# Optimization experiments

Measured on AMD Instinct MI355X. Metric: run time of the kernel, lower is better.

The kernel has to match this reference:

```python
import jax, jax.numpy as jnp
import numpy as np

B, S, D, V = 4, 512, 512, 32000
GAMMA = 0.5
EPS = 1e-12  # torch F.normalize clamp_min eps


def _l2norm(x, axis):
    n = jnp.sqrt(jnp.sum(x * x, axis=axis, keepdims=True))
    return x / jnp.maximum(n, EPS)


def setup_inputs() -> dict:
    key = jax.random.key(0)
    k1, k2, k3 = jax.random.split(key, 3)
    preds = jax.random.normal(k1, (B, D, S), dtype=jnp.float32)
    emb_weight = jax.random.normal(k2, (V, D), dtype=jnp.float32)
    target = jax.random.randint(k3, (B, S), 0, V, dtype=jnp.int64)
    return {"preds": preds, "emb_weight": emb_weight, "target": target, "pad_id": 0}


def reference(preds, emb_weight, target, pad_id):
    # preds: [B, D, S] -> [B, S, D], L2-normalized over D
    out_norm = _l2norm(jnp.transpose(preds, (0, 2, 1)), axis=2)
    voc_norm = _l2norm(emb_weight, axis=1)          # [V, D]
    tgt_emb = emb_weight[target]                     # [B, S, D] (raw lookup, not normalized)
    mask = target != pad_id                          # [B, S]

    cos_out_voc = jnp.einsum('bsd,vd->bsv', out_norm, voc_norm)  # [B, S, V]
    tgt_voc = jnp.einsum('bsd,vd->bsv', tgt_emb, voc_norm)       # [B, S, V]

    jmax = jnp.argmax(cos_out_voc - tgt_voc, axis=2)             # [B, S]
    cos_target = jnp.take_along_axis(cos_out_voc, target[..., None], axis=2)[..., 0]
    max_cos_voc = jnp.take_along_axis(cos_out_voc, jmax[..., None], axis=2)[..., 0]

    diff = jnp.maximum(GAMMA + max_cos_voc - cos_target, 0.0)    # [B, S]
    denom = jnp.sum(mask).astype(diff.dtype)
    return jnp.sum(jnp.where(mask, diff, 0.0)) / denom
```

## Files before the change

### kernel.cpp

```cpp
#include <hip/hip_runtime.h>
#include <math.h>


#define Bb 4
#define Ss 512
#define Dd 512
#define Vv 32000
#define ROWS (Bb * Ss)
#define NTILE_M (ROWS / 128)
#define NTILE_N (Vv / 128)
#define VOC_BLOCKS (Vv / 4)

typedef __attribute__((ext_vector_type(8))) short bf16x8;
typedef __attribute__((ext_vector_type(4))) float f32x4;

__device__ __forceinline__ float waveReduceSum(float x) {
#pragma unroll
  for (int m = 32; m >= 1; m >>= 1) x += __shfl_xor(x, m, 64);
  return x;
}

__device__ __forceinline__ unsigned short f2bf(float f) {
  unsigned u = __float_as_uint(f);
  unsigned r = (u + 0x7FFFu + ((u >> 16) & 1u)) >> 16;
  return (unsigned short)r;
}

__device__ __forceinline__ unsigned long long packSC(float s, int c) {
  unsigned b = __float_as_uint(s);
  unsigned key = b ^ ((b & 0x80000000u) ? 0xFFFFFFFFu : 0x80000000u);
  return ((unsigned long long)key << 32) | (unsigned)(~c);
}

__device__ __forceinline__ void async_ld16(const void* g, void* l) {
  __builtin_amdgcn_global_load_lds((const __attribute__((address_space(1))) void*)g,
                                   (__attribute__((address_space(3))) void*)l, 16, 0, 0);
}

__global__ __launch_bounds__(256) void prep_all(
    const float* __restrict__ preds, const float* __restrict__ emb,
    const int* __restrict__ target,
    float* __restrict__ o_rows, short* __restrict__ u_bf,
    float* __restrict__ cos_tgt, short* __restrict__ ebf,
    float* __restrict__ inv_norm) {
  int tid = threadIdx.x;
  int wave = tid >> 6, lane = tid & 63;
  if (blockIdx.x < VOC_BLOCKS) {
    int v = blockIdx.x * 4 + wave;
    const float* e = emb + (size_t)v * Dd;
    float4 x0 = *(const float4*)(e + lane * 8);
    float4 x1 = *(const float4*)(e + lane * 8 + 4);
    float ss = x0.x * x0.x + x0.y * x0.y + x0.z * x0.z + x0.w * x0.w +
               x1.x * x1.x + x1.y * x1.y + x1.z * x1.z + x1.w * x1.w;
    ss = waveReduceSum(ss);
    float inv = 1.0f / fmaxf(sqrtf(ss), 1e-12f);
    bf16x8 o;
    o[0] = (short)f2bf(x0.x * inv); o[1] = (short)f2bf(x0.y * inv);
    o[2] = (short)f2bf(x0.z * inv); o[3] = (short)f2bf(x0.w * inv);
    o[4] = (short)f2bf(x1.x * inv); o[5] = (short)f2bf(x1.y * inv);
    o[6] = (short)f2bf(x1.z * inv); o[7] = (short)f2bf(x1.w * inv);
    *(bf16x8*)(ebf + (size_t)v * Dd + lane * 8) = o;
    if (lane == 0) inv_norm[v] = inv;
  } else {
    int row = blockIdx.x - VOC_BLOCKS;
    int b = row >> 9, s = row & (Ss - 1);
    const float* p = preds + (size_t)b * Dd * Ss + s;
    float x0 = p[(size_t)tid * Ss];
    float x1 = p[(size_t)(tid + 256) * Ss];
    __shared__ float red[12];
    float ss = waveReduceSum(x0 * x0 + x1 * x1);
    if (lane == 0) red[wave] = ss;
    __syncthreads();
    float inv = 1.0f / fmaxf(sqrtf(red[0] + red[1] + red[2] + red[3]), 1e-12f);
    float o0 = x0 * inv, o1 = x1 * inv;
    o_rows[(size_t)row * Dd + tid] = o0;
    o_rows[(size_t)row * Dd + tid + 256] = o1;
    int t = target[row];
    const float* et = emb + (size_t)t * Dd;
    float e0 = et[tid], e1 = et[tid + 256];
    u_bf[(size_t)row * Dd + tid] = (short)f2bf(o0 - e0);
    u_bf[(size_t)row * Dd + tid + 256] = (short)f2bf(o1 - e1);
    float ss2 = waveReduceSum(e0 * e0 + e1 * e1);
    float dt = waveReduceSum(o0 * e0 + o1 * e1);
    if (lane == 0) { red[4 + wave] = ss2; red[8 + wave] = dt; }
    __syncthreads();
    if (tid == 0) {
      float n2 = red[4] + red[5] + red[6] + red[7];
      float dd = red[8] + red[9] + red[10] + red[11];
      cos_tgt[row] = dd * (1.0f / fmaxf(sqrtf(n2), 1e-12f));
    }
  }
}

__global__ __launch_bounds__(256, 4) void gemm_argmax(
    const short* __restrict__ u_bf, const short* __restrict__ ebf,
    unsigned long long* __restrict__ part) {
  __shared__ short sA[128 * 64];
  __shared__ short sB[128 * 64];
  int bid = blockIdx.x;
  int g = (bid & 7) * 500 + (bid >> 3);
  int tm = g & 15, tn = g >> 4;
  int tid = threadIdx.x;
  int w = tid >> 6, lane = tid & 63;
  int wm = w >> 1, wn = w & 1;

  int srow = w * 8 + (lane >> 3);
  int schunk = (lane & 7) ^ ((lane >> 3) & 7);
  const short* gA = u_bf + (size_t)(tm * 128 + srow) * Dd + schunk * 8;
  const short* gB = ebf + (size_t)(tn * 128 + srow) * Dd + schunk * 8;

  int fr = lane & 15;
  int q = lane >> 4;
  int ck0 = ((q) ^ (fr & 7)) * 8;
  int ck1 = ((4 + q) ^ (fr & 7)) * 8;

  f32x4 acc[4][4];
  f32x4 z = {0.f, 0.f, 0.f, 0.f};
#pragma unroll
  for (int mi = 0; mi < 4; ++mi)
#pragma unroll
    for (int ni = 0; ni < 4; ++ni) acc[mi][ni] = z;

  for (int kk = 0; kk < Dd / 64; ++kk) {
    __syncthreads();
    {
      const short* ga = gA + kk * 64;
      const short* gb = gB + kk * 64;
#pragma unroll
      for (int i = 0; i < 4; ++i) {
        async_ld16(ga + (size_t)(i * 32) * Dd, &sA[(w * 8 + i * 32) * 64]);
        async_ld16(gb + (size_t)(i * 32) * Dd, &sB[(w * 8 + i * 32) * 64]);
      }
    }
    __syncthreads();
    bf16x8 af[4], bg[4];
#pragma unroll
    for (int mi = 0; mi < 4; ++mi)
      af[mi] = *(const bf16x8*)(sA + (wm * 64 + mi * 16 + fr) * 64 + ck0);
#pragma unroll
    for (int ni = 0; ni < 4; ++ni)
      bg[ni] = *(const bf16x8*)(sB + (wn * 64 + ni * 16 + fr) * 64 + ck0);
#pragma unroll
    for (int mi = 0; mi < 4; ++mi)
#pragma unroll
      for (int ni = 0; ni < 4; ++ni)
        acc[mi][ni] = __builtin_amdgcn_mfma_f32_16x16x32_bf16(af[mi], bg[ni], acc[mi][ni], 0, 0, 0);
#pragma unroll
    for (int mi = 0; mi < 4; ++mi)
      af[mi] = *(const bf16x8*)(sA + (wm * 64 + mi * 16 + fr) * 64 + ck1);
#pragma unroll
    for (int ni = 0; ni < 4; ++ni)
      bg[ni] = *(const bf16x8*)(sB + (wn * 64 + ni * 16 + fr) * 64 + ck1);
#pragma unroll
    for (int mi = 0; mi < 4; ++mi)
#pragma unroll
      for (int ni = 0; ni < 4; ++ni)
        acc[mi][ni] = __builtin_amdgcn_mfma_f32_16x16x32_bf16(af[mi], bg[ni], acc[mi][ni], 0, 0, 0);
  }

  float bs[4][4];
  int bc[4][4];
  int col0 = tn * 128 + wn * 64 + (lane & 15);
#pragma unroll
  for (int mi = 0; mi < 4; ++mi) {
#pragma unroll
    for (int j = 0; j < 4; ++j) { bs[mi][j] = acc[mi][0][j]; bc[mi][j] = col0; }
#pragma unroll
    for (int ni = 1; ni < 4; ++ni) {
      int c = col0 + ni * 16;
#pragma unroll
      for (int j = 0; j < 4; ++j) {
        float v = acc[mi][ni][j];
        if (v > bs[mi][j]) { bs[mi][j] = v; bc[mi][j] = c; }
      }
    }
  }
#pragma unroll
  for (int m = 1; m < 16; m <<= 1) {
#pragma unroll
    for (int mi = 0; mi < 4; ++mi)
#pragma unroll
      for (int j = 0; j < 4; ++j) {
        float os = __shfl_xor(bs[mi][j], m, 64);
        int oc = __shfl_xor(bc[mi][j], m, 64);
        if (os > bs[mi][j] || (os == bs[mi][j] && oc < bc[mi][j])) {
          bs[mi][j] = os;
          bc[mi][j] = oc;
        }
      }
  }
  __syncthreads();
  float* sEs = (float*)sA;
  int* sEc = (int*)sA + 256;
  if ((lane & 15) == 0) {
    int qq = lane >> 4;
#pragma unroll
    for (int mi = 0; mi < 4; ++mi)
#pragma unroll
      for (int j = 0; j < 4; ++j) {
        int rloc = wm * 64 + mi * 16 + qq * 4 + j;
        sEs[wn * 128 + rloc] = bs[mi][j];
        sEc[wn * 128 + rloc] = bc[mi][j];
      }
  }
  __syncthreads();
  if (tid < 128) {
    float s0 = sEs[tid], s1 = sEs[128 + tid];
    int c0 = sEc[tid], c1 = sEc[128 + tid];
    if (s1 > s0 || (s1 == s0 && c1 < c0)) { s0 = s1; c0 = c1; }
    part[(size_t)tn * ROWS + tm * 128 + tid] = packSC(s0, c0);
  }
}

__global__ __launch_bounds__(256) void row_final(
    const float* __restrict__ o_rows, const float* __restrict__ emb,
    const float* __restrict__ inv_norm, const float* __restrict__ cos_tgt,
    const int* __restrict__ target, const int* __restrict__ pad_id,
    const unsigned long long* __restrict__ part, float* __restrict__ diffs) {
  int wave = threadIdx.x >> 6, lane = threadIdx.x & 63;
  int row = blockIdx.x * 4 + wave;
  unsigned long long best = 0ull;
  for (int t = lane; t < NTILE_N; t += 64) {
    unsigned long long p = part[(size_t)t * ROWS + row];
    if (p > best) best = p;
  }
#pragma unroll
  for (int m = 1; m < 64; m <<= 1) {
    unsigned long long o = __shfl_xor(best, m, 64);
    if (o > best) best = o;
  }
  int bi = (int)(~(unsigned)(best & 0xFFFFFFFFull));
  const float* o = o_rows + (size_t)row * Dd;
  const float* e = emb + (size_t)bi * Dd;
  float d = 0.f;
#pragma unroll
  for (int i = 0; i < Dd / 64; ++i) d += o[lane + 64 * i] * e[lane + 64 * i];
  d = waveReduceSum(d);
  if (lane == 0) {
    float cmax = d * inv_norm[bi];
    int t = target[row];
    float df = fmaxf(0.5f + cmax - cos_tgt[row], 0.0f);
    diffs[row] = (t != pad_id[0]) ? df : 0.0f;
  }
}

__global__ __launch_bounds__(256) void reduce_final(
    const float* __restrict__ diffs, const int* __restrict__ target,
    const int* __restrict__ pad_id, float* __restrict__ out) {
  int tid = threadIdx.x;
  int pid = pad_id[0];
  float s = 0.f, c = 0.f;
  for (int i = tid; i < ROWS; i += 256) {
    s += diffs[i];
    c += (target[i] != pid) ? 1.0f : 0.0f;
  }
  s = waveReduceSum(s);
  c = waveReduceSum(c);
  __shared__ float rs[4], rc[4];
  int wave = tid >> 6, lane = tid & 63;
  if (lane == 0) { rs[wave] = s; rc[wave] = c; }
  __syncthreads();
  if (tid == 0) out[0] = (rs[0] + rs[1] + rs[2] + rs[3]) / (rc[0] + rc[1] + rc[2] + rc[3]);
}

extern "C" void kernel_launch(void* const* d_in, const int* in_sizes, int n_in,
                              void* d_out, int out_size, void* d_ws, size_t ws_size,
                              hipStream_t stream) {
  const float* preds = (const float*)d_in[0];
  const float* emb = (const float*)d_in[1];
  const int* target = (const int*)d_in[2];
  const int* pad_id = (const int*)d_in[3];
  char* ws = (char*)d_ws;
  float* o_rows = (float*)ws;
  short* u_bf = (short*)(ws + 4194304);
  short* ebf = (short*)(ws + 6291456);
  float* inv_norm = (float*)(ws + 39059456);
  float* cos_tgt = (float*)(ws + 39187456);
  unsigned long long* part = (unsigned long long*)(ws + 39195648);
  float* diffs = (float*)(ws + 43291648);

  prep_all<<<VOC_BLOCKS + ROWS, 256, 0, stream>>>(preds, emb, target, o_rows, u_bf,
                                                  cos_tgt, ebf, inv_norm);
  gemm_argmax<<<NTILE_M * NTILE_N, 256, 0, stream>>>(u_bf, ebf, part);
  row_final<<<ROWS / 4, 256, 0, stream>>>(o_rows, emb, inv_norm, cos_tgt, target,
                                          pad_id, part, diffs);
  reduce_final<<<1, 256, 0, stream>>>(diffs, target, pad_id, (float*)d_out);
}
```

Measured before the change: 206.8 us.

## Switch argmax GEMM to FP8 with exact FP32 rescoring of near-max candidates

Quantizes the normalized vocabulary and the difference vectors to FP8 e4m3 and runs the scoring GEMM with fp8 MFMA instructions. This halves GEMM operand bytes and raises matrix throughput. To make up for the lost precision, row_final gathers the per-tile maxima within a margin of the global max and recomputes each candidate's score exactly in FP32 before choosing the argmax. The cost is more work in row_final and a per-row serial loop over 250 tiles, plus a risk of missing the true argmax if FP8 error exceeds the margin.

```diff
diff --git a/kernel.cpp b/kernel.cpp
--- a/kernel.cpp
+++ b/kernel.cpp
@@ -11,7 +11,6 @@
 #define NTILE_N (Vv / 128)
 #define VOC_BLOCKS (Vv / 4)
 
-typedef __attribute__((ext_vector_type(8))) short bf16x8;
 typedef __attribute__((ext_vector_type(4))) float f32x4;
 
 __device__ __forceinline__ float waveReduceSum(float x) {
@@ -20,16 +19,15 @@
   return x;
 }
 
-__device__ __forceinline__ unsigned short f2bf(float f) {
-  unsigned u = __float_as_uint(f);
-  unsigned r = (u + 0x7FFFu + ((u >> 16) & 1u)) >> 16;
-  return (unsigned short)r;
-}
-
-__device__ __forceinline__ unsigned long long packSC(float s, int c) {
-  unsigned b = __float_as_uint(s);
-  unsigned key = b ^ ((b & 0x80000000u) ? 0xFFFFFFFFu : 0x80000000u);
-  return ((unsigned long long)key << 32) | (unsigned)(~c);
+__device__ __forceinline__ float waveReduceMax(float x) {
+#pragma unroll
+  for (int m = 32; m >= 1; m >>= 1) x = fmaxf(x, __shfl_xor(x, m, 64));
+  return x;
+}
+
+__device__ __forceinline__ unsigned char f2e4m3(float f) {
+  int p = __builtin_amdgcn_cvt_pk_fp8_f32(f, f, 0, false);
+  return (unsigned char)(p & 0xff);
 }
 
 __device__ __forceinline__ void async_ld16(const void* g, void* l) {
@@ -40,8 +38,8 @@
 __global__ __launch_bounds__(256) void prep_all(
     const float* __restrict__ preds, const float* __restrict__ emb,
     const int* __restrict__ target,
-    float* __restrict__ o_rows, short* __restrict__ u_bf,
-    float* __restrict__ cos_tgt, short* __restrict__ ebf,
+    float* __restrict__ o_rows, unsigned char* __restrict__ u8,
+    float* __restrict__ cos_tgt, unsigned char* __restrict__ e8,
     float* __restrict__ inv_norm) {
   int tid = threadIdx.x;
   int wave = tid >> 6, lane = tid & 63;
@@ -54,12 +52,12 @@
                x1.x * x1.x + x1.y * x1.y + x1.z * x1.z + x1.w * x1.w;
     ss = waveReduceSum(ss);
     float inv = 1.0f / fmaxf(sqrtf(ss), 1e-12f);
-    bf16x8 o;
-    o[0] = (short)f2bf(x0.x * inv); o[1] = (short)f2bf(x0.y * inv);
-    o[2] = (short)f2bf(x0.z * inv); o[3] = (short)f2bf(x0.w * inv);
-    o[4] = (short)f2bf(x1.x * inv); o[5] = (short)f2bf(x1.y * inv);
-    o[6] = (short)f2bf(x1.z * inv); o[7] = (short)f2bf(x1.w * inv);
-    *(bf16x8*)(ebf + (size_t)v * Dd + lane * 8) = o;
+    int lo = __builtin_amdgcn_cvt_pk_fp8_f32(x0.x * inv, x0.y * inv, 0, false);
+    lo = __builtin_amdgcn_cvt_pk_fp8_f32(x0.z * inv, x0.w * inv, lo, true);
+    int hi = __builtin_amdgcn_cvt_pk_fp8_f32(x1.x * inv, x1.y * inv, 0, false);
+    hi = __builtin_amdgcn_cvt_pk_fp8_f32(x1.z * inv, x1.w * inv, hi, true);
+    int2 pk = make_int2(lo, hi);
+    *(int2*)(e8 + (size_t)v * Dd + lane * 8) = pk;
     if (lane == 0) inv_norm[v] = inv;
   } else {
     int row = blockIdx.x - VOC_BLOCKS;
@@ -78,8 +76,8 @@
     int t = target[row];
     const float* et = emb + (size_t)t * Dd;
     float e0 = et[tid], e1 = et[tid + 256];
-    u_bf[(size_t)row * Dd + tid] = (short)f2bf(o0 - e0);
-    u_bf[(size_t)row * Dd + tid + 256] = (short)f2bf(o1 - e1);
+    u8[(size_t)row * Dd + tid] = f2e4m3(o0 - e0);
+    u8[(size_t)row * Dd + tid + 256] = f2e4m3(o1 - e1);
     float ss2 = waveReduceSum(e0 * e0 + e1 * e1);
     float dt = waveReduceSum(o0 * e0 + o1 * e1);
     if (lane == 0) { red[4 + wave] = ss2; red[8 + wave] = dt; }
@@ -93,10 +91,10 @@
 }
 
 __global__ __launch_bounds__(256, 4) void gemm_argmax(
-    const short* __restrict__ u_bf, const short* __restrict__ ebf,
-    unsigned long long* __restrict__ part) {
-  __shared__ short sA[128 * 64];
-  __shared__ short sB[128 * 64];
+    const unsigned char* __restrict__ u8, const unsigned char* __restrict__ e8,
+    float* __restrict__ part_s, int* __restrict__ part_i) {
+  __shared__ unsigned char sA[128 * 128];
+  __shared__ unsigned char sB[128 * 128];
   int bid = blockIdx.x;
   int g = (bid & 7) * 500 + (bid >> 3);
   int tm = g & 15, tn = g >> 4;
@@ -106,13 +104,13 @@
 
   int srow = w * 8 + (lane >> 3);
   int schunk = (lane & 7) ^ ((lane >> 3) & 7);
-  const short* gA = u_bf + (size_t)(tm * 128 + srow) * Dd + schunk * 8;
-  const short* gB = ebf + (size_t)(tn * 128 + srow) * Dd + schunk * 8;
+  const unsigned char* gA = u8 + (size_t)(tm * 128 + srow) * Dd + schunk * 16;
+  const unsigned char* gB = e8 + (size_t)(tn * 128 + srow) * Dd + schunk * 16;
 
   int fr = lane & 15;
   int q = lane >> 4;
-  int ck0 = ((q) ^ (fr & 7)) * 8;
-  int ck1 = ((4 + q) ^ (fr & 7)) * 8;
+  int qh = q >> 1, ql = (q & 1) * 8;
+  int flow = fr & 7;
 
   f32x4 acc[4][4];
   f32x4 z = {0.f, 0.f, 0.f, 0.f};
@@ -121,41 +119,34 @@
 #pragma unroll
     for (int ni = 0; ni < 4; ++ni) acc[mi][ni] = z;
 
-  for (int kk = 0; kk < Dd / 64; ++kk) {
+  for (int kk = 0; kk < 4; ++kk) {
     __syncthreads();
     {
-      const short* ga = gA + kk * 64;
-      const short* gb = gB + kk * 64;
+      const unsigned char* ga = gA + kk * 128;
+      const unsigned char* gb = gB + kk * 128;
 #pragma unroll
       for (int i = 0; i < 4; ++i) {
-        async_ld16(ga + (size_t)(i * 32) * Dd, &sA[(w * 8 + i * 32) * 64]);
-        async_ld16(gb + (size_t)(i * 32) * Dd, &sB[(w * 8 + i * 32) * 64]);
+        async_ld16(ga + (size_t)(i * 32) * Dd, &sA[(w * 8 + i * 32) * 128]);
+        async_ld16(gb + (size_t)(i * 32) * Dd, &sB[(w * 8 + i * 32) * 128]);
       }
     }
     __syncthreads();
-    bf16x8 af[4], bg[4];
-#pragma unroll
-    for (int mi = 0; mi < 4; ++mi)
-      af[mi] = *(const bf16x8*)(sA + (wm * 64 + mi * 16 + fr) * 64 + ck0);
-#pragma unroll
-    for (int ni = 0; ni < 4; ++ni)
-      bg[ni] = *(const bf16x8*)(sB + (wn * 64 + ni * 16 + fr) * 64 + ck0);
-#pragma unroll
-    for (int mi = 0; mi < 4; ++mi)
+#pragma unroll
+    for (int kc = 0; kc < 4; ++kc) {
+      int off = ((2 * kc + qh) ^ flow) * 16 + ql;
+      long af[4], bg[4];
+#pragma unroll
+      for (int mi = 0; mi < 4; ++mi)
+        af[mi] = *(const long*)(sA + (wm * 64 + mi * 16 + fr) * 128 + off);
 #pragma unroll
       for (int ni = 0; ni < 4; ++ni)
-        acc[mi][ni] = __builtin_amdgcn_mfma_f32_16x16x32_bf16(af[mi], bg[ni], acc[mi][ni], 0, 0, 0);
-#pragma unroll
-    for (int mi = 0; mi < 4; ++mi)
-      af[mi] = *(const bf16x8*)(sA + (wm * 64 + mi * 16 + fr) * 64 + ck1);
-#pragma unroll
-    for (int ni = 0; ni < 4; ++ni)
-      bg[ni] = *(const bf16x8*)(sB + (wn * 64 + ni * 16 + fr) * 64 + ck1);
-#pragma unroll
-    for (int mi = 0; mi < 4; ++mi)
-#pragma unroll
-      for (int ni = 0; ni < 4; ++ni)
-        acc[mi][ni] = __builtin_amdgcn_mfma_f32_16x16x32_bf16(af[mi], bg[ni], acc[mi][ni], 0, 0, 0);
+        bg[ni] = *(const long*)(sB + (wn * 64 + ni * 16 + fr) * 128 + off);
+#pragma unroll
+      for (int mi = 0; mi < 4; ++mi)
+#pragma unroll
+        for (int ni = 0; ni < 4; ++ni)
+          acc[mi][ni] = __builtin_amdgcn_mfma_f32_16x16x32_fp8_fp8(af[mi], bg[ni], acc[mi][ni], 0, 0, 0);
+    }
   }
 
   float bs[4][4];
@@ -208,39 +199,61 @@
     float s0 = sEs[tid], s1 = sEs[128 + tid];
     int c0 = sEc[tid], c1 = sEc[128 + tid];
     if (s1 > s0 || (s1 == s0 && c1 < c0)) { s0 = s1; c0 = c1; }
-    part[(size_t)tn * ROWS + tm * 128 + tid] = packSC(s0, c0);
-  }
-}
-
+    part_s[(size_t)tn * ROWS + tm * 128 + tid] = s0;
+    part_i[(size_t)tn * ROWS + tm * 128 + tid] = c0;
+  }
+}
+
+#define MARGIN 0.5f
 __global__ __launch_bounds__(256) void row_final(
     const float* __restrict__ o_rows, const float* __restrict__ emb,
     const float* __restrict__ inv_norm, const float* __restrict__ cos_tgt,
     const int* __restrict__ target, const int* __restrict__ pad_id,
-    const unsigned long long* __restrict__ part, float* __restrict__ diffs) {
+    const float* __restrict__ part_s, const int* __restrict__ part_i,
+    float* __restrict__ diffs) {
   int wave = threadIdx.x >> 6, lane = threadIdx.x & 63;
   int row = blockIdx.x * 4 + wave;
-  unsigned long long best = 0ull;
-  for (int t = lane; t < NTILE_N; t += 64) {
-    unsigned long long p = part[(size_t)t * ROWS + row];
-    if (p > best) best = p;
-  }
-#pragma unroll
-  for (int m = 1; m < 64; m <<= 1) {
-    unsigned long long o = __shfl_xor(best, m, 64);
-    if (o > best) best = o;
-  }
-  int bi = (int)(~(unsigned)(best & 0xFFFFFFFFull));
+  int tgt = target[row];
   const float* o = o_rows + (size_t)row * Dd;
-  const float* e = emb + (size_t)bi * Dd;
-  float d = 0.f;
-#pragma unroll
-  for (int i = 0; i < Dd / 64; ++i) d += o[lane + 64 * i] * e[lane + 64 * i];
-  d = waveReduceSum(d);
+  const float* et = emb + (size_t)tgt * Dd;
+  float4 oa = *(const float4*)(o + lane * 8);
+  float4 ob = *(const float4*)(o + lane * 8 + 4);
+  float4 ta = *(const float4*)(et + lane * 8);
+  float4 tb = *(const float4*)(et + lane * 8 + 4);
+
+  float m = -INFINITY;
+  for (int t = lane; t < NTILE_N; t += 64) m = fmaxf(m, part_s[(size_t)t * ROWS + row]);
+  m = waveReduceMax(m);
+  float thr = m - MARGIN;
+
+  float bscore = -INFINITY;
+  int bcol = 0x7fffffff;
+  float bdo = 0.f;
+  for (int t = 0; t < NTILE_N; ++t) {
+    float s8 = part_s[(size_t)t * ROWS + row];
+    if (s8 >= thr) {
+      int c = part_i[(size_t)t * ROWS + row];
+      const float* ec = emb + (size_t)c * Dd;
+      float4 ea = *(const float4*)(ec + lane * 8);
+      float4 eb = *(const float4*)(ec + lane * 8 + 4);
+      float po = oa.x * ea.x + oa.y * ea.y + oa.z * ea.z + oa.w * ea.w +
+                 ob.x * eb.x + ob.y * eb.y + ob.z * eb.z + ob.w * eb.w;
+      float pt = ta.x * ea.x + ta.y * ea.y + ta.z * ea.z + ta.w * ea.w +
+                 tb.x * eb.x + tb.y * eb.y + tb.z * eb.z + tb.w * eb.w;
+      po = waveReduceSum(po);
+      pt = waveReduceSum(pt);
+      float sc = (po - pt) * inv_norm[c];
+      if (sc > bscore || (sc == bscore && c < bcol)) {
+        bscore = sc;
+        bcol = c;
+        bdo = po;
+      }
+    }
+  }
   if (lane == 0) {
-    float cmax = d * inv_norm[bi];
-    int t = target[row];
+    float cmax = bdo * inv_norm[bcol];
     float df = fmaxf(0.5f + cmax - cos_tgt[row], 0.0f);
-    diffs[row] = (t != pad_id[0]) ? df : 0.0f;
+    diffs[row] = (tgt != pad_id[0]) ? df : 0.0f;
   }
 }
 
@@ -272,17 +285,18 @@
   const int* pad_id = (const int*)d_in[3];
   char* ws = (char*)d_ws;
   float* o_rows = (float*)ws;
-  short* u_bf = (short*)(ws + 4194304);
-  short* ebf = (short*)(ws + 6291456);
-  float* inv_norm = (float*)(ws + 39059456);
-  float* cos_tgt = (float*)(ws + 39187456);
-  unsigned long long* part = (unsigned long long*)(ws + 39195648);
-  float* diffs = (float*)(ws + 43291648);
-
-  prep_all<<<VOC_BLOCKS + ROWS, 256, 0, stream>>>(preds, emb, target, o_rows, u_bf,
-                                                  cos_tgt, ebf, inv_norm);
-  gemm_argmax<<<NTILE_M * NTILE_N, 256, 0, stream>>>(u_bf, ebf, part);
+  unsigned char* u8 = (unsigned char*)(ws + 4194304);
+  unsigned char* e8 = (unsigned char*)(ws + 5242880);
+  float* inv_norm = (float*)(ws + 21626880);
+  float* cos_tgt = (float*)(ws + 21754880);
+  float* part_s = (float*)(ws + 21763072);
+  int* part_i = (int*)(ws + 23811072);
+  float* diffs = (float*)(ws + 25859072);
+
+  prep_all<<<VOC_BLOCKS + ROWS, 256, 0, stream>>>(preds, emb, target, o_rows, u8,
+                                                  cos_tgt, e8, inv_norm);
+  gemm_argmax<<<NTILE_M * NTILE_N, 256, 0, stream>>>(u8, e8, part_s, part_i);
   row_final<<<ROWS / 4, 256, 0, stream>>>(o_rows, emb, inv_norm, cos_tgt, target,
-                                          pad_id, part, diffs);
+                                          pad_id, part_s, part_i, diffs);
   reduce_final<<<1, 256, 0, stream>>>(diffs, target, pad_id, (float*)d_out);
 }
```

Measured after the change: 255.1 us. 1.23x slower.
